# Kernel tuning notes

Measured on AMD Instinct MI355X. Metric: run time of the kernel, lower is better.

## Reference

```python
import jax, jax.numpy as jnp
import numpy as np

B, S, D_MODEL, D_ATTN = 4, 2048, 1024, 1024
NEG_INF = jnp.float32(-jnp.inf)


def setup_inputs() -> dict:
    key = jax.random.key(0)
    ks = jax.random.split(key, 6)
    scale = 1.0 / np.sqrt(D_MODEL)
    return {
        "x": jax.random.normal(ks[0], (B, S, D_MODEL), dtype=jnp.float32),
        "mask": jnp.ones((B, S), dtype=jnp.float32),
        "Wq": jax.random.normal(ks[1], (D_ATTN, D_MODEL), dtype=jnp.float32) * scale,
        "Wk": jax.random.normal(ks[2], (D_ATTN, D_MODEL), dtype=jnp.float32) * scale,
        "Wv": jax.random.normal(ks[3], (D_ATTN, D_MODEL), dtype=jnp.float32) * scale,
        "Wo": jax.random.normal(ks[4], (D_MODEL, D_ATTN), dtype=jnp.float32) * scale,
        "bo": jnp.zeros((D_MODEL,), dtype=jnp.float32),
    }


def reference(x, mask, Wq, Wk, Wv, Wo, bo):
    # x: [B,S,Dm]; torch Linear weight is [out,in], so y = x @ W.T
    q = jnp.einsum("bsd,ad->bsa", x, Wq)  # [B,S,Da]
    k = jnp.einsum("bsd,ad->bsa", x, Wk)
    v = jnp.einsum("bsd,ad->bsa", x, Wv)  # NOTE: v from x (original quirk)
    logits = jnp.einsum("bqa,bka->bqk", q, k)  # [B,S,S]
    # causal mask (cross_attention=True path): keep lower triangle incl. diag
    causal = jnp.tril(jnp.ones((S, S), dtype=bool))
    logits = jnp.where(causal[None], logits, NEG_INF)
    # padding mask: outer product of per-token mask
    square_mask = mask[:, :, None] * mask[:, None, :]  # [B,S,S]
    logits = jnp.where(square_mask == 1, logits, NEG_INF)
    # scale by sqrt(d_model) AFTER masking (as in original)
    attn = jax.nn.softmax(logits / jnp.sqrt(jnp.float32(D_MODEL)), axis=-1)
    attn_out = jnp.einsum("bqk,bka->bqa", attn, v)  # [B,S,Da]
    return jnp.einsum("bsa,da->bsd", attn_out, Wo) + bo
```

## Files before the change

### kernel.cpp

```cpp
#include <hip/hip_runtime.h>
#include <hip/hip_bf16.h>
#include <cstdio>

typedef __bf16 bf16x8 __attribute__((ext_vector_type(8)));
typedef float f32x4 __attribute__((ext_vector_type(4)));

#define BM 128
#define BN 128
#define BK 64

__device__ __forceinline__ unsigned short f2bf(float f) {
  union { float f; unsigned u; } v; v.f = f;
  unsigned u = v.u;
  return (unsigned short)((u + 0x7FFFu + ((u >> 16) & 1u)) >> 16);
}

__device__ __forceinline__ float bf2f(unsigned short s) {
  union { unsigned u; float f; } v; v.u = ((unsigned)s) << 16;
  return v.f;
}

#define GLOAD16(gsrc, ldst) \
  __builtin_amdgcn_global_load_lds((const __attribute__((address_space(1))) void*)(gsrc), \
                                   (__attribute__((address_space(3))) void*)(ldst), 16, 0, 0)

template<int EPI>
__global__ __launch_bounds__(256, 3)
void gemm_bt(const unsigned short* __restrict__ A, const unsigned short* __restrict__ B,
             void* __restrict__ Cv, void* __restrict__ Cv2, void* __restrict__ Cv3,
             const float* __restrict__ bias,
             int K, int ldA, int ldB, int ldC,
             long aBat, long bBat, long cBat,
             int causalSkip, int causalKlim, float scale, int revM)
{
  const int gx = gridDim.x;
  const int nwg = gx * gridDim.y;
  const int flat = blockIdx.y * gx + blockIdx.x;
  const int qch = nwg >> 3, rch = nwg & 7;
  const int xcd = flat & 7, idx = flat >> 3;
  const int swz = (xcd < rch ? xcd * (qch + 1) : rch * (qch + 1) + (xcd - rch) * qch) + idx;
  const int bx = swz % gx;
  int by = swz / gx;
  if (revM) by = gridDim.y - 1 - by;

  const int m0 = by * BM;
  const int n0 = bx * BN;
  if (causalSkip && n0 > m0) return;
  const int bz = blockIdx.z;

  const unsigned short* Ab = A + (long)bz * aBat + (long)m0 * ldA;
  const unsigned short* Bb = B + (long)bz * bBat + (long)n0 * ldB;

  __shared__ short lds[2][BM * BK];

  const int tid = threadIdx.x;
  const int lane = tid & 63;
  const int wave = tid >> 6;
  const int wr = wave >> 1, wc = wave & 1;

  const int Keff = causalKlim ? min(K, m0 + BM) : K;
  const int nk = Keff / BK;

  const int srow = tid >> 3;
  const int sch = tid & 7;

  const f32x4 fzero = {0.f, 0.f, 0.f, 0.f};
  f32x4 acc[4][4];
#pragma unroll
  for (int i = 0; i < 4; i++)
#pragma unroll
    for (int j = 0; j < 4; j++) acc[i][j] = fzero;

  int aOff[4][2], bOff[4][2];
#pragma unroll
  for (int i = 0; i < 4; i++) {
#pragma unroll
    for (int s = 0; s < 2; s++) {
      int ra = wr * 64 + i * 16 + (lane & 15);
      aOff[i][s] = ra * BK + (((s * 4 + (lane >> 4)) ^ (ra & 7)) * 8);
      int rb = wc * 64 + i * 16 + (lane & 15);
      bOff[i][s] = rb * BK + (((s * 4 + (lane >> 4)) ^ (rb & 7)) * 8);
    }
  }

  for (int kt = 0; kt < nk; kt++) {
    const unsigned short* Ak = Ab + kt * BK;
    const unsigned short* Bk = Bb + kt * BK;
#pragma unroll
    for (int r = 0; r < 4; r++) {
      int row = r * 32 + srow;
      int sc = sch ^ (row & 7);
      GLOAD16(Ak + (long)row * ldA + sc * 8, &lds[0][(r * 32 + wave * 8) * BK]);
    }
#pragma unroll
    for (int r = 0; r < 4; r++) {
      int row = r * 32 + srow;
      int sc = sch ^ (row & 7);
      GLOAD16(Bk + (long)row * ldB + sc * 8, &lds[1][(r * 32 + wave * 8) * BK]);
    }
    __syncthreads();

#pragma unroll
    for (int s = 0; s < 2; s++) {
      bf16x8 av[4], bv[4];
#pragma unroll
      for (int i = 0; i < 4; i++) av[i] = *reinterpret_cast<const bf16x8*>(lds[0] + aOff[i][s]);
#pragma unroll
      for (int j = 0; j < 4; j++) bv[j] = *reinterpret_cast<const bf16x8*>(lds[1] + bOff[j][s]);
#pragma unroll
      for (int i = 0; i < 4; i++)
#pragma unroll
        for (int j = 0; j < 4; j++)
          acc[i][j] = __builtin_amdgcn_mfma_f32_16x16x32_bf16(av[i], bv[j], acc[i][j], 0, 0, 0);
    }
    __syncthreads();
  }

  const int rb4 = (lane >> 4) * 4;
  const int cl = lane & 15;
#pragma unroll
  for (int i = 0; i < 4; i++) {
#pragma unroll
    for (int j = 0; j < 4; j++) {
      const int gm = m0 + wr * 64 + i * 16 + rb4;
      const int gn = n0 + wc * 64 + j * 16 + cl;
      if (EPI == 0) {
        unsigned short* C = (unsigned short*)Cv + (long)bz * cBat;
#pragma unroll
        for (int r = 0; r < 4; r++)
          C[(long)(gm + r) * ldC + gn] = f2bf(acc[i][j][r] * scale);
      } else if (EPI == 2) {
        float* C = (float*)Cv;
        const float bb = bias[gn];
#pragma unroll
        for (int r = 0; r < 4; r++)
          C[(long)(gm + r) * ldC + gn] = acc[i][j][r] + bb;
      } else if (EPI == 4) {
        if (gn < 1024) {
          unsigned short* C = (unsigned short*)Cv;
#pragma unroll
          for (int r = 0; r < 4; r++)
            C[(long)(gm + r) * 1024 + gn] = f2bf(acc[i][j][r]);
        } else if (gn < 2048) {
          unsigned short* C = (unsigned short*)Cv2;
#pragma unroll
          for (int r = 0; r < 4; r++)
            C[(long)(gm + r) * 1024 + (gn - 1024)] = f2bf(acc[i][j][r]);
        } else {
          const int d = gn - 2048;
          const int b = gm >> 11;
          const int sIdx = gm & 2047;
          unsigned short* C = (unsigned short*)Cv3 + (long)b * (2048L * 1024)
                              + (long)d * 2048 + sIdx;
          ushort4 pk;
          pk.x = f2bf(acc[i][j][0]);
          pk.y = f2bf(acc[i][j][1]);
          pk.z = f2bf(acc[i][j][2]);
          pk.w = f2bf(acc[i][j][3]);
          *reinterpret_cast<ushort4*>(C) = pk;
        }
      }
    }
  }
}

__global__ __launch_bounds__(256)
void softmax_rows(const unsigned short* __restrict__ Sb, const float* __restrict__ maskv,
                  unsigned short* __restrict__ P, int Sdim)
{
  const int q = blockIdx.x;
  const int b = blockIdx.y;
  const int kmax = (q & ~127) + 128;
  const unsigned short* row = Sb + ((long)b * Sdim + q) * Sdim;
  unsigned short* prow = P + ((long)b * Sdim + q) * Sdim;
  const float* mrow = maskv + (long)b * Sdim;
  const int tid = threadIdx.x;
  const float mq = mrow[q];
  const int k0 = tid * 8;
  const bool live = (k0 < kmax);

  float v[8];
  if (live) {
    uint4 raw = *reinterpret_cast<const uint4*>(row + k0);
    const unsigned short* us = reinterpret_cast<const unsigned short*>(&raw);
    float4 ma = *reinterpret_cast<const float4*>(mrow + k0);
    float4 mb = *reinterpret_cast<const float4*>(mrow + k0 + 4);
    float mv[8] = {ma.x, ma.y, ma.z, ma.w, mb.x, mb.y, mb.z, mb.w};
#pragma unroll
    for (int u = 0; u < 8; u++) {
      const int k = k0 + u;
      const bool ok = (k <= q) && (mq * mv[u] == 1.0f);
      v[u] = ok ? bf2f(us[u]) : -INFINITY;
    }
  } else {
#pragma unroll
    for (int u = 0; u < 8; u++) v[u] = -INFINITY;
  }

  float mx = -INFINITY;
#pragma unroll
  for (int u = 0; u < 8; u++) mx = fmaxf(mx, v[u]);
#pragma unroll
  for (int o = 32; o; o >>= 1) mx = fmaxf(mx, __shfl_xor(mx, o));
  __shared__ float redm[4], reds[4];
  if ((tid & 63) == 0) redm[tid >> 6] = mx;
  __syncthreads();
  mx = fmaxf(fmaxf(redm[0], redm[1]), fmaxf(redm[2], redm[3]));

  float p[8];
  float sm = 0.f;
#pragma unroll
  for (int u = 0; u < 8; u++) {
    p[u] = (v[u] > -INFINITY) ? __expf(v[u] - mx) : 0.f;
    sm += p[u];
  }
#pragma unroll
  for (int o = 32; o; o >>= 1) sm += __shfl_xor(sm, o);
  if ((tid & 63) == 0) reds[tid >> 6] = sm;
  __syncthreads();
  sm = reds[0] + reds[1] + reds[2] + reds[3];
  const float inv = 1.0f / sm;

  if (live) {
    union { unsigned short us[8]; uint4 u4; } pk;
#pragma unroll
    for (int u = 0; u < 8; u++) pk.us[u] = f2bf(p[u] * inv);
    *reinterpret_cast<uint4*>(prow + k0) = pk.u4;
  }
}

__global__ __launch_bounds__(256)
void cast_all(const float* __restrict__ x, const float* __restrict__ w0,
              const float* __restrict__ w1, const float* __restrict__ w2,
              const float* __restrict__ w3,
              unsigned short* __restrict__ xb, unsigned short* __restrict__ dqkv,
              unsigned short* __restrict__ dout)
{
  const int blk = blockIdx.x;
  const float* src;
  unsigned short* dst;
  int i;
  if (blk < 4096) {
    src = x; dst = xb; i = (blk * 256 + threadIdx.x) * 8;
  } else {
    const int w = (blk - 4096) >> 9;
    const int off = (blk - 4096) & 511;
    src = (w == 0) ? w0 : (w == 1) ? w1 : (w == 2) ? w2 : w3;
    dst = (w < 3) ? (dqkv + (long)w * 1024 * 1024) : dout;
    i = (off * 256 + threadIdx.x) * 8;
  }
  float4 a = *reinterpret_cast<const float4*>(src + i);
  float4 b = *reinterpret_cast<const float4*>(src + i + 4);
  union { unsigned short us[8]; uint4 u4; } pk;
  pk.us[0] = f2bf(a.x); pk.us[1] = f2bf(a.y); pk.us[2] = f2bf(a.z); pk.us[3] = f2bf(a.w);
  pk.us[4] = f2bf(b.x); pk.us[5] = f2bf(b.y); pk.us[6] = f2bf(b.z); pk.us[7] = f2bf(b.w);
  *reinterpret_cast<uint4*>(dst + i) = pk.u4;
}

extern "C" void kernel_launch(void* const* d_in, const int* in_sizes, int n_in,
                              void* d_out, int out_size, void* d_ws, size_t ws_size,
                              hipStream_t stream)
{
  const int B = 4, S = 2048, D = 1024;
  const float* x  = (const float*)d_in[0];
  const float* mk = (const float*)d_in[1];
  const float* Wq = (const float*)d_in[2];
  const float* Wk = (const float*)d_in[3];
  const float* Wv = (const float*)d_in[4];
  const float* Wo = (const float*)d_in[5];
  const float* bo = (const float*)d_in[6];
  float* out = (float*)d_out;

  char* ws = (char*)d_ws;
  const long MB = 1024L * 1024L;
  unsigned short* Xbf  = (unsigned short*)(ws + 0);
  unsigned short* Qb   = (unsigned short*)(ws + 16 * MB);
  unsigned short* Kb   = (unsigned short*)(ws + 32 * MB);
  unsigned short* Vt   = (unsigned short*)(ws + 48 * MB);
  unsigned short* Wqkv = (unsigned short*)(ws + 64 * MB);
  unsigned short* Wob  = (unsigned short*)(ws + 70 * MB);
  unsigned short* Sbuf = (unsigned short*)(ws + 72 * MB);
  unsigned short* P    = Qb;
  unsigned short* O    = Xbf;

  if (ws_size < (size_t)(104 * MB)) {
    fprintf(stderr, "kernel_launch: ws too small (%zu bytes, need 104MB)\n", ws_size);
    return;
  }

  cast_all<<<dim3(4096 + 2048), 256, 0, stream>>>(x, Wq, Wk, Wv, Wo, Xbf, Wqkv, Wob);

  const dim3 blk(256);
  dim3 gQKV(3072 / BN, 8192 / BM, 1);
  gemm_bt<4><<<gQKV, blk, 0, stream>>>(Xbf, Wqkv, Qb, Kb, Vt, nullptr,
                                       1024, 1024, 1024, 0,
                                       0, 0, 0, 0, 0, 1.0f, 0);
  dim3 gS(2048 / BN, 2048 / BM, 4);
  gemm_bt<0><<<gS, blk, 0, stream>>>(Qb, Kb, Sbuf, nullptr, nullptr, nullptr,
                                     1024, 1024, 1024, 2048,
                                     (long)S * 1024, (long)S * 1024, (long)S * S,
                                     1, 0, 0.03125f, 0);
  softmax_rows<<<dim3(2048, 4), blk, 0, stream>>>(Sbuf, mk, P, 2048);
  dim3 gO(1024 / BN, 2048 / BM, 4);
  gemm_bt<0><<<gO, blk, 0, stream>>>(P, Vt, O, nullptr, nullptr, nullptr,
                                     2048, 2048, 2048, 1024,
                                     (long)S * S, (long)D * S, (long)S * D,
                                     0, 1, 1.0f, 1);
  dim3 gF(1024 / BN, 8192 / BM, 1);
  gemm_bt<2><<<gF, blk, 0, stream>>>(O, Wob, out, nullptr, nullptr, bo,
                                     1024, 1024, 1024, 1024,
                                     0, 0, 0, 0, 0, 1.0f, 0);
}
```

Baseline: 183.0 us.

## Add double-buffered LDS GEMM for PV and output projection; wave-per-row softmax

Adds a new gemm_db kernel that keeps two LDS stages of A/B tiles and prefetches tile k+2 while computing on the current tile. It uses explicit waitcnt and barrier scheduling plus raised priority around the MFMA block, and is applied to the P·V and output-projection GEMMs. Separately, softmax now processes one row per wave (4 rows per block), which removes the cross-wave LDS reductions and __syncthreads. The cost is doubled LDS use (occupancy bound lowered to 2) and more fragile hand-scheduled synchronisation.

```diff
diff --git a/kernel.cpp b/kernel.cpp
--- a/kernel.cpp
+++ b/kernel.cpp
@@ -26,12 +26,11 @@
 
 template<int EPI>
 __global__ __launch_bounds__(256, 3)
-void gemm_bt(const unsigned short* __restrict__ A, const unsigned short* __restrict__ B,
+void gemm_sb(const unsigned short* __restrict__ A, const unsigned short* __restrict__ B,
              void* __restrict__ Cv, void* __restrict__ Cv2, void* __restrict__ Cv3,
-             const float* __restrict__ bias,
              int K, int ldA, int ldB, int ldC,
              long aBat, long bBat, long cBat,
-             int causalSkip, int causalKlim, float scale, int revM)
+             int causalSkip, float scale)
 {
   const int gx = gridDim.x;
   const int nwg = gx * gridDim.y;
@@ -40,8 +39,7 @@
   const int xcd = flat & 7, idx = flat >> 3;
   const int swz = (xcd < rch ? xcd * (qch + 1) : rch * (qch + 1) + (xcd - rch) * qch) + idx;
   const int bx = swz % gx;
-  int by = swz / gx;
-  if (revM) by = gridDim.y - 1 - by;
+  const int by = swz / gx;
 
   const int m0 = by * BM;
   const int n0 = bx * BN;
@@ -58,8 +56,7 @@
   const int wave = tid >> 6;
   const int wr = wave >> 1, wc = wave & 1;
 
-  const int Keff = causalKlim ? min(K, m0 + BM) : K;
-  const int nk = Keff / BK;
+  const int nk = K / BK;
 
   const int srow = tid >> 3;
   const int sch = tid & 7;
@@ -129,13 +126,7 @@
 #pragma unroll
         for (int r = 0; r < 4; r++)
           C[(long)(gm + r) * ldC + gn] = f2bf(acc[i][j][r] * scale);
-      } else if (EPI == 2) {
-        float* C = (float*)Cv;
-        const float bb = bias[gn];
-#pragma unroll
-        for (int r = 0; r < 4; r++)
-          C[(long)(gm + r) * ldC + gn] = acc[i][j][r] + bb;
-      } else if (EPI == 4) {
+      } else {
         if (gn < 1024) {
           unsigned short* C = (unsigned short*)Cv;
 #pragma unroll
@@ -164,68 +155,212 @@
   }
 }
 
+template<int EPI>
+__global__ __launch_bounds__(256, 2)
+void gemm_db(const unsigned short* __restrict__ A, const unsigned short* __restrict__ B,
+             void* __restrict__ Cv, const float* __restrict__ bias,
+             int K, int ldA, int ldB, int ldC,
+             long aBat, long bBat, long cBat,
+             int causalKlim, float scale, int revM)
+{
+  const int gx = gridDim.x;
+  const int nwg = gx * gridDim.y;
+  const int flat = blockIdx.y * gx + blockIdx.x;
+  const int qch = nwg >> 3, rch = nwg & 7;
+  const int xcd = flat & 7, idx = flat >> 3;
+  const int swz = (xcd < rch ? xcd * (qch + 1) : rch * (qch + 1) + (xcd - rch) * qch) + idx;
+  const int bx = swz % gx;
+  int by = swz / gx;
+  if (revM) by = gridDim.y - 1 - by;
+
+  const int m0 = by * BM;
+  const int n0 = bx * BN;
+  const int bz = blockIdx.z;
+
+  const unsigned short* Ab = A + (long)bz * aBat + (long)m0 * ldA;
+  const unsigned short* Bb = B + (long)bz * bBat + (long)n0 * ldB;
+
+  __shared__ short lds[2][2][BM * BK];
+
+  const int tid = threadIdx.x;
+  const int lane = tid & 63;
+  const int wave = tid >> 6;
+  const int wr = wave >> 1, wc = wave & 1;
+
+  const int Keff = causalKlim ? min(K, m0 + BM) : K;
+  const int nk = Keff / BK;
+
+  const int srow = tid >> 3;
+  const int sch = tid & 7;
+
+  const f32x4 fzero = {0.f, 0.f, 0.f, 0.f};
+  f32x4 acc[4][4];
+#pragma unroll
+  for (int i = 0; i < 4; i++)
+#pragma unroll
+    for (int j = 0; j < 4; j++) acc[i][j] = fzero;
+
+  int aOff[4][2], bOff[4][2];
+#pragma unroll
+  for (int i = 0; i < 4; i++) {
+#pragma unroll
+    for (int s = 0; s < 2; s++) {
+      int ra = wr * 64 + i * 16 + (lane & 15);
+      aOff[i][s] = ra * BK + (((s * 4 + (lane >> 4)) ^ (ra & 7)) * 8);
+      int rb = wc * 64 + i * 16 + (lane & 15);
+      bOff[i][s] = rb * BK + (((s * 4 + (lane >> 4)) ^ (rb & 7)) * 8);
+    }
+  }
+
+  auto stage = [&](int buf, int kt) {
+    const unsigned short* Ak = Ab + kt * BK;
+    const unsigned short* Bk = Bb + kt * BK;
+#pragma unroll
+    for (int r = 0; r < 4; r++) {
+      int row = r * 32 + srow;
+      int sc = sch ^ (row & 7);
+      GLOAD16(Ak + (long)row * ldA + sc * 8, &lds[buf][0][(r * 32 + wave * 8) * BK]);
+    }
+#pragma unroll
+    for (int r = 0; r < 4; r++) {
+      int row = r * 32 + srow;
+      int sc = sch ^ (row & 7);
+      GLOAD16(Bk + (long)row * ldB + sc * 8, &lds[buf][1][(r * 32 + wave * 8) * BK]);
+    }
+  };
+
+  stage(0, 0);
+  stage(1, 1);
+  asm volatile("s_waitcnt vmcnt(8)" ::: "memory");
+  __builtin_amdgcn_sched_barrier(0);
+  __builtin_amdgcn_s_barrier();
+
+  int cur = 0;
+  for (int kt = 0; kt < nk; kt++) {
+    const short* La = lds[cur][0];
+    const short* Lb = lds[cur][1];
+    bf16x8 av[2][4], bv[2][4];
+#pragma unroll
+    for (int s = 0; s < 2; s++) {
+#pragma unroll
+      for (int i = 0; i < 4; i++) {
+        av[s][i] = *reinterpret_cast<const bf16x8*>(La + aOff[i][s]);
+        bv[s][i] = *reinterpret_cast<const bf16x8*>(Lb + bOff[i][s]);
+      }
+    }
+    asm volatile("s_waitcnt lgkmcnt(0)" ::: "memory");
+    __builtin_amdgcn_sched_barrier(0);
+    __builtin_amdgcn_s_barrier();
+    __builtin_amdgcn_sched_barrier(0);
+
+    if (kt + 2 < nk) {
+      stage(cur, kt + 2);
+      asm volatile("s_waitcnt vmcnt(8)" ::: "memory");
+    } else if (kt + 1 < nk) {
+      asm volatile("s_waitcnt vmcnt(0)" ::: "memory");
+    }
+    if (kt + 1 < nk) {
+      __builtin_amdgcn_s_barrier();
+      __builtin_amdgcn_sched_barrier(0);
+    }
+
+    __builtin_amdgcn_s_setprio(1);
+#pragma unroll
+    for (int s = 0; s < 2; s++)
+#pragma unroll
+      for (int i = 0; i < 4; i++)
+#pragma unroll
+        for (int j = 0; j < 4; j++)
+          acc[i][j] = __builtin_amdgcn_mfma_f32_16x16x32_bf16(av[s][i], bv[s][j], acc[i][j], 0, 0, 0);
+    __builtin_amdgcn_s_setprio(0);
+    __builtin_amdgcn_sched_barrier(0);
+    cur ^= 1;
+  }
+
+  const int rb4 = (lane >> 4) * 4;
+  const int cl = lane & 15;
+#pragma unroll
+  for (int i = 0; i < 4; i++) {
+#pragma unroll
+    for (int j = 0; j < 4; j++) {
+      const int gm = m0 + wr * 64 + i * 16 + rb4;
+      const int gn = n0 + wc * 64 + j * 16 + cl;
+      if (EPI == 0) {
+        unsigned short* C = (unsigned short*)Cv + (long)bz * cBat;
+#pragma unroll
+        for (int r = 0; r < 4; r++)
+          C[(long)(gm + r) * ldC + gn] = f2bf(acc[i][j][r] * scale);
+      } else {
+        float* C = (float*)Cv;
+        const float bb = bias[gn];
+#pragma unroll
+        for (int r = 0; r < 4; r++)
+          C[(long)(gm + r) * ldC + gn] = acc[i][j][r] + bb;
+      }
+    }
+  }
+}
+
 __global__ __launch_bounds__(256)
 void softmax_rows(const unsigned short* __restrict__ Sb, const float* __restrict__ maskv,
                   unsigned short* __restrict__ P, int Sdim)
 {
-  const int q = blockIdx.x;
+  const int wv = threadIdx.x >> 6;
+  const int lane = threadIdx.x & 63;
+  const int q = blockIdx.x * 4 + wv;
   const int b = blockIdx.y;
   const int kmax = (q & ~127) + 128;
   const unsigned short* row = Sb + ((long)b * Sdim + q) * Sdim;
   unsigned short* prow = P + ((long)b * Sdim + q) * Sdim;
   const float* mrow = maskv + (long)b * Sdim;
-  const int tid = threadIdx.x;
   const float mq = mrow[q];
-  const int k0 = tid * 8;
-  const bool live = (k0 < kmax);
-
-  float v[8];
-  if (live) {
-    uint4 raw = *reinterpret_cast<const uint4*>(row + k0);
-    const unsigned short* us = reinterpret_cast<const unsigned short*>(&raw);
-    float4 ma = *reinterpret_cast<const float4*>(mrow + k0);
-    float4 mb = *reinterpret_cast<const float4*>(mrow + k0 + 4);
-    float mv[8] = {ma.x, ma.y, ma.z, ma.w, mb.x, mb.y, mb.z, mb.w};
+
+  float v[4][8];
+  float mx = -INFINITY;
+#pragma unroll
+  for (int c = 0; c < 4; c++) {
+    const int k0 = c * 512 + lane * 8;
+    if (c * 512 < kmax) {
+      uint4 raw = *reinterpret_cast<const uint4*>(row + k0);
+      const unsigned short* us = reinterpret_cast<const unsigned short*>(&raw);
+      float4 ma = *reinterpret_cast<const float4*>(mrow + k0);
+      float4 mb = *reinterpret_cast<const float4*>(mrow + k0 + 4);
+      float mv[8] = {ma.x, ma.y, ma.z, ma.w, mb.x, mb.y, mb.z, mb.w};
+#pragma unroll
+      for (int u = 0; u < 8; u++) {
+        const int k = k0 + u;
+        const bool ok = (k <= q) && (mq * mv[u] == 1.0f);
+        v[c][u] = ok ? bf2f(us[u]) : -INFINITY;
+        mx = fmaxf(mx, v[c][u]);
+      }
+    } else {
+#pragma unroll
+      for (int u = 0; u < 8; u++) v[c][u] = -INFINITY;
+    }
+  }
+#pragma unroll
+  for (int o = 32; o; o >>= 1) mx = fmaxf(mx, __shfl_xor(mx, o));
+
+  float sm = 0.f;
+#pragma unroll
+  for (int c = 0; c < 4; c++)
 #pragma unroll
     for (int u = 0; u < 8; u++) {
-      const int k = k0 + u;
-      const bool ok = (k <= q) && (mq * mv[u] == 1.0f);
-      v[u] = ok ? bf2f(us[u]) : -INFINITY;
-    }
-  } else {
-#pragma unroll
-    for (int u = 0; u < 8; u++) v[u] = -INFINITY;
-  }
-
-  float mx = -INFINITY;
-#pragma unroll
-  for (int u = 0; u < 8; u++) mx = fmaxf(mx, v[u]);
-#pragma unroll
-  for (int o = 32; o; o >>= 1) mx = fmaxf(mx, __shfl_xor(mx, o));
-  __shared__ float redm[4], reds[4];
-  if ((tid & 63) == 0) redm[tid >> 6] = mx;
-  __syncthreads();
-  mx = fmaxf(fmaxf(redm[0], redm[1]), fmaxf(redm[2], redm[3]));
-
-  float p[8];
-  float sm = 0.f;
-#pragma unroll
-  for (int u = 0; u < 8; u++) {
-    p[u] = (v[u] > -INFINITY) ? __expf(v[u] - mx) : 0.f;
-    sm += p[u];
-  }
+      v[c][u] = (v[c][u] > -INFINITY) ? __expf(v[c][u] - mx) : 0.f;
+      sm += v[c][u];
+    }
 #pragma unroll
   for (int o = 32; o; o >>= 1) sm += __shfl_xor(sm, o);
-  if ((tid & 63) == 0) reds[tid >> 6] = sm;
-  __syncthreads();
-  sm = reds[0] + reds[1] + reds[2] + reds[3];
   const float inv = 1.0f / sm;
 
-  if (live) {
-    union { unsigned short us[8]; uint4 u4; } pk;
-#pragma unroll
-    for (int u = 0; u < 8; u++) pk.us[u] = f2bf(p[u] * inv);
-    *reinterpret_cast<uint4*>(prow + k0) = pk.u4;
+#pragma unroll
+  for (int c = 0; c < 4; c++) {
+    if (c * 512 < kmax) {
+      union { unsigned short us[8]; uint4 u4; } pk;
+#pragma unroll
+      for (int u = 0; u < 8; u++) pk.us[u] = f2bf(v[c][u] * inv);
+      *reinterpret_cast<uint4*>(prow + c * 512 + lane * 8) = pk.u4;
+    }
   }
 }
 
@@ -292,22 +427,22 @@
 
   const dim3 blk(256);
   dim3 gQKV(3072 / BN, 8192 / BM, 1);
-  gemm_bt<4><<<gQKV, blk, 0, stream>>>(Xbf, Wqkv, Qb, Kb, Vt, nullptr,
+  gemm_sb<4><<<gQKV, blk, 0, stream>>>(Xbf, Wqkv, Qb, Kb, Vt,
                                        1024, 1024, 1024, 0,
-                                       0, 0, 0, 0, 0, 1.0f, 0);
+                                       0, 0, 0, 0, 1.0f);
   dim3 gS(2048 / BN, 2048 / BM, 4);
-  gemm_bt<0><<<gS, blk, 0, stream>>>(Qb, Kb, Sbuf, nullptr, nullptr, nullptr,
+  gemm_sb<0><<<gS, blk, 0, stream>>>(Qb, Kb, Sbuf, nullptr, nullptr,
                                      1024, 1024, 1024, 2048,
                                      (long)S * 1024, (long)S * 1024, (long)S * S,
-                                     1, 0, 0.03125f, 0);
-  softmax_rows<<<dim3(2048, 4), blk, 0, stream>>>(Sbuf, mk, P, 2048);
+                                     1, 0.03125f);
+  softmax_rows<<<dim3(512, 4), blk, 0, stream>>>(Sbuf, mk, P, 2048);
   dim3 gO(1024 / BN, 2048 / BM, 4);
-  gemm_bt<0><<<gO, blk, 0, stream>>>(P, Vt, O, nullptr, nullptr, nullptr,
+  gemm_db<0><<<gO, blk, 0, stream>>>(P, Vt, O, nullptr,
                                      2048, 2048, 2048, 1024,
                                      (long)S * S, (long)D * S, (long)S * D,
-                                     0, 1, 1.0f, 1);
+                                     1, 1.0f, 1);
   dim3 gF(1024 / BN, 8192 / BM, 1);
-  gemm_bt<2><<<gF, blk, 0, stream>>>(O, Wob, out, nullptr, nullptr, bo,
+  gemm_db<2><<<gF, blk, 0, stream>>>(O, Wob, out, bo,
                                      1024, 1024, 1024, 1024,
-                                     0, 0, 0, 0, 0, 1.0f, 0);
-}
+                                     0, 0, 0, 0, 1.0f, 0);
+}
```

Measured after the change: 175.4 us. -4.1%, faster.
